# Optimization experiments

Hardware: AMD Instinct MI355X
Metric: run time of the kernel (lower is better)

Reference implementation:

```python
import jax, jax.numpy as jnp
import numpy as np

B = 256          # games in flight
BS = 19          # board side
N2 = BS * BS     # 361 points
M = N2 * 10      # history_factor = 10 -> max moves = 3610


def setup_inputs() -> dict:
    key = jax.random.key(0)
    k = jax.random.split(key, 8)
    legal_mask = jax.random.bernoulli(k[0], 0.5, (B, BS, BS))
    # captures are sparse: few stones captured per candidate move
    capture_stone_mask = jax.random.bernoulli(k[1], 0.02, (B, N2, N2))
    current_player = jax.random.randint(k[2], (B,), 0, 2, dtype=jnp.int32)
    zpos = jax.random.randint(k[3], (N2, 3), 0, 2**31 - 1, dtype=jnp.int32)
    current_hash = jax.random.randint(k[4], (B,), 0, 2**31 - 1, dtype=jnp.int32)
    hash_history = jax.random.randint(k[5], (B, M), 0, 2**31 - 1, dtype=jnp.int32)
    move_count = jax.random.randint(k[6], (B,), 0, M, dtype=jnp.int32)
    logits = jax.random.normal(k[7], (B, BS, BS), dtype=jnp.float32)
    return dict(legal_mask=legal_mask, capture_stone_mask=capture_stone_mask,
                current_player=current_player, zpos=zpos,
                current_hash=current_hash, hash_history=hash_history,
                move_count=move_count, logits=logits)


def _super_ko_filter(legal_mask, capture_stone_mask, current_player, zpos,
                     current_hash, hash_history, move_count):
    Bb, H, W = legal_mask.shape
    n2 = H * W
    legal_flat = legal_mask.reshape(Bb, n2)                      # (B, N2)
    player = current_player.astype(jnp.int32)                    # (B,)
    zposT = zpos.T                                               # (3, N2)

    # 1) delta for placing the stone: empty-key XOR player-key
    place_old = zposT[0][None, :]                                # (1, N2)
    place_new = zposT[player + 1]                                # (B, N2) gather per-batch
    place_delta = jnp.bitwise_xor(place_old, place_new)          # (B, N2)

    # 2) delta for removing a captured opponent stone at each point
    z_opp = zposT[2 - player]                                    # opp+1 = 2-player, (B, N2)
    D = jnp.bitwise_xor(z_opp, zposT[0][None, :])                # (B, N2)

    # per candidate move, XOR the deltas of all stones it would capture
    sel = jnp.where(capture_stone_mask, D[:, None, :], jnp.int32(0))  # (B, N2, N2)
    cap_delta = jax.lax.reduce(sel, jnp.int32(0), jax.lax.bitwise_xor, (2,))  # (B, N2)

    # 3) post-move hash per candidate
    new_hash = current_hash[:, None] ^ place_delta ^ cap_delta   # (B, N2)

    # 4) reject if post-move hash appears in the (valid prefix of) history
    hist_mask = jnp.arange(hash_history.shape[1])[None, :] < move_count[:, None]  # (B, M)
    eq = (new_hash[:, :, None] == hash_history[:, None, :]) & hist_mask[:, None, :]
    is_repeat = jnp.any(eq, axis=2) & legal_flat                 # (B, N2)

    return legal_mask & ~is_repeat.reshape(Bb, H, W)


def reference(legal_mask, capture_stone_mask, current_player, zpos,
              current_hash, hash_history, move_count, logits):
    final_mask = _super_ko_filter(legal_mask, capture_stone_mask, current_player,
                                  zpos, current_hash, hash_history, move_count)
    # downstream use of the filtered mask: mask policy logits
    return jnp.where(final_mask, logits, jnp.float32(-1e9))
```

## Files before the change

### kernel.cpp

```cpp
#include <hip/hip_runtime.h>
#include <stdint.h>


#define GO_B     256
#define GO_N2    361
#define GO_M     3610
#define GO_SLABB (GO_N2 * GO_N2 * 4)
#define TBL      1024
#define NTHR     1024
#define DEPTH    8

__global__ __launch_bounds__(NTHR)
void superko_kernel(const int*   __restrict__ legal,
                    const int*   __restrict__ cap,
                    const int*   __restrict__ player,
                    const int*   __restrict__ zpos,
                    const int*   __restrict__ chash,
                    const int*   __restrict__ hist,
                    const int*   __restrict__ mcount,
                    const float* __restrict__ logits,
                    float*       __restrict__ out)
{
    __shared__ uint32_t Dl[GO_N2];
    __shared__ uint32_t capx[GO_N2];
    __shared__ uint32_t pd[GO_N2];
    __shared__ uint32_t thash[TBL];
    __shared__ int      tidx[TBL];
    __shared__ uint8_t  rep[GO_N2];
    __shared__ uint8_t  leg[GO_N2];

    const int b   = blockIdx.x;
    const int tid = threadIdx.x;
    const int p   = player[b];

    for (int i = tid; i < GO_N2; i += NTHR) {
        uint32_t z0 = (uint32_t)zpos[i * 3 + 0];
        uint32_t zp = (uint32_t)zpos[i * 3 + 1 + p];
        uint32_t zo = (uint32_t)zpos[i * 3 + 2 - p];
        Dl[i]   = zo ^ z0;
        pd[i]   = z0 ^ zp;
        capx[i] = 0u;
        rep[i]  = 0u;
        leg[i]  = legal[(size_t)b * GO_N2 + i] != 0;
    }
    for (int s = tid; s < TBL; s += NTHR) tidx[s] = -1;
    __syncthreads();

    {
        uintptr_t p0   = (uintptr_t)cap + (size_t)b * GO_SLABB;
        uintptr_t a0   = p0 & ~(uintptr_t)15;
        const uint32_t lead   = (uint32_t)(p0 - a0);
        const uint32_t nchunk = (lead + GO_SLABB + 15u) >> 4;
        const uint4* __restrict__ src = (const uint4*)a0;

        for (uint32_t cb = 0; cb < nchunk; cb += NTHR * DEPTH) {
            uint4 w[DEPTH];
            #pragma unroll
            for (int k = 0; k < DEPTH; ++k) {
                uint32_t c = cb + (uint32_t)tid + (uint32_t)k * NTHR;
                uint4 z; z.x = 0u; z.y = 0u; z.z = 0u; z.w = 0u;
                w[k] = (c < nchunk) ? src[c] : z;
            }
            #pragma unroll
            for (int k = 0; k < DEPTH; ++k) {
                uint4 ww = w[k];
                if ((ww.x | ww.y | ww.z | ww.w) == 0u) continue;
                uint32_t base = (cb + (uint32_t)tid + (uint32_t)k * NTHR) * 16u - lead;
                uint32_t dw[4] = { ww.x, ww.y, ww.z, ww.w };
                #pragma unroll
                for (int d = 0; d < 4; ++d) {
                    if (dw[d] != 0u) {
                        uint32_t f = base + (uint32_t)(d * 4);
                        if (f < (uint32_t)GO_SLABB) {
                            uint32_t e = f >> 2;
                            uint32_t i = e / 361u;
                            uint32_t j = e - i * 361u;
                            atomicXor(&capx[i], Dl[j]);
                        }
                    }
                }
            }
        }
    }
    __syncthreads();

    const uint32_t ch = (uint32_t)chash[b];
    for (int i = tid; i < GO_N2; i += NTHR) {
        uint32_t nh = ch ^ pd[i] ^ capx[i];
        if (leg[i]) {
            uint32_t s = nh & (TBL - 1);
            while (true) {
                int prev = atomicCAS(&tidx[s], -1, i);
                if (prev == -1) { thash[s] = nh; break; }
                s = (s + 1) & (TBL - 1);
            }
        }
    }
    __syncthreads();

    const int mc = mcount[b];
    for (int m = tid; m < mc; m += NTHR) {
        uint32_t h = (uint32_t)hist[(size_t)b * GO_M + m];
        uint32_t s = h & (TBL - 1);
        while (tidx[s] != -1) {
            if (thash[s] == h) rep[tidx[s]] = 1u;
            s = (s + 1) & (TBL - 1);
        }
    }
    __syncthreads();

    for (int i = tid; i < GO_N2; i += NTHR) {
        bool keep = leg[i] && !rep[i];
        out[(size_t)b * GO_N2 + i] =
            keep ? logits[(size_t)b * GO_N2 + i] : -1.0e9f;
    }
}

extern "C" void kernel_launch(void* const* d_in, const int* in_sizes, int n_in,
                              void* d_out, int out_size, void* d_ws, size_t ws_size,
                              hipStream_t stream) {
    const int*   legal  = (const int*)d_in[0];
    const int*   cap    = (const int*)d_in[1];
    const int*   player = (const int*)d_in[2];
    const int*   zpos   = (const int*)d_in[3];
    const int*   chash  = (const int*)d_in[4];
    const int*   hist   = (const int*)d_in[5];
    const int*   mcount = (const int*)d_in[6];
    const float* logits = (const float*)d_in[7];
    float*       outp   = (float*)d_out;

    superko_kernel<<<GO_B, NTHR, 0, stream>>>(legal, cap, player, zpos, chash,
                                              hist, mcount, logits, outp);
}
```

Before: 216.8 us.

## Split capture-mask scan across four blocks per game with separate finalize kernel

Each game's capture slab is now scanned by four smaller blocks writing partial XOR accumulators to workspace. A second kernel combines the partials, builds the hash table and checks history. This is meant to raise occupancy and memory-level parallelism beyond one block per game. It adds a second launch and a workspace round-trip.

```diff
diff --git a/kernel.cpp b/kernel.cpp
--- a/kernel.cpp
+++ b/kernel.cpp
@@ -6,24 +6,88 @@
 #define GO_N2    361
 #define GO_M     3610
 #define GO_SLABB (GO_N2 * GO_N2 * 4)
+#define NSPLIT   4
+#define ATHR     512
+#define BTHR     512
 #define TBL      1024
-#define NTHR     1024
 #define DEPTH    8
 
-__global__ __launch_bounds__(NTHR)
-void superko_kernel(const int*   __restrict__ legal,
-                    const int*   __restrict__ cap,
-                    const int*   __restrict__ player,
-                    const int*   __restrict__ zpos,
-                    const int*   __restrict__ chash,
-                    const int*   __restrict__ hist,
-                    const int*   __restrict__ mcount,
-                    const float* __restrict__ logits,
-                    float*       __restrict__ out)
+__global__ __launch_bounds__(ATHR, 8)
+void scan_kernel(const int* __restrict__ cap,
+                 const int* __restrict__ player,
+                 const int* __restrict__ zpos,
+                 uint32_t*  __restrict__ partial)
 {
     __shared__ uint32_t Dl[GO_N2];
     __shared__ uint32_t capx[GO_N2];
-    __shared__ uint32_t pd[GO_N2];
+
+    const int b   = blockIdx.x >> 2;
+    const int q   = blockIdx.x & 3;
+    const int tid = threadIdx.x;
+    const int p   = player[b];
+
+    for (int i = tid; i < GO_N2; i += ATHR) {
+        uint32_t z0 = (uint32_t)zpos[i * 3 + 0];
+        uint32_t zo = (uint32_t)zpos[i * 3 + 2 - p];
+        Dl[i]   = zo ^ z0;
+        capx[i] = 0u;
+    }
+    __syncthreads();
+
+    uintptr_t p0   = (uintptr_t)cap + (size_t)b * GO_SLABB;
+    uintptr_t a0   = p0 & ~(uintptr_t)15;
+    const uint32_t lead   = (uint32_t)(p0 - a0);
+    const uint32_t nchunk = (lead + GO_SLABB + 15u) >> 4;
+    const uint32_t nq     = (nchunk + NSPLIT - 1) / NSPLIT;
+    const uint32_t c0     = (uint32_t)q * nq;
+    const uint32_t c1     = (c0 + nq < nchunk) ? (c0 + nq) : nchunk;
+    const uint4* __restrict__ src = (const uint4*)a0;
+
+    for (uint32_t cb = c0; cb < c1; cb += ATHR * DEPTH) {
+        uint4 w[DEPTH];
+        #pragma unroll
+        for (int k = 0; k < DEPTH; ++k) {
+            uint32_t c = cb + (uint32_t)tid + (uint32_t)k * ATHR;
+            uint4 z; z.x = 0u; z.y = 0u; z.z = 0u; z.w = 0u;
+            w[k] = (c < c1) ? src[c] : z;
+        }
+        #pragma unroll
+        for (int k = 0; k < DEPTH; ++k) {
+            uint4 ww = w[k];
+            if ((ww.x | ww.y | ww.z | ww.w) == 0u) continue;
+            uint32_t base = (cb + (uint32_t)tid + (uint32_t)k * ATHR) * 16u - lead;
+            uint32_t dw[4] = { ww.x, ww.y, ww.z, ww.w };
+            #pragma unroll
+            for (int d = 0; d < 4; ++d) {
+                if (dw[d] != 0u) {
+                    uint32_t f = base + (uint32_t)(d * 4);
+                    if (f < (uint32_t)GO_SLABB) {
+                        uint32_t e = f >> 2;
+                        uint32_t i = e / 361u;
+                        uint32_t j = e - i * 361u;
+                        atomicXor(&capx[i], Dl[j]);
+                    }
+                }
+            }
+        }
+    }
+    __syncthreads();
+
+    uint32_t* __restrict__ dst = partial + ((size_t)b * NSPLIT + q) * GO_N2;
+    for (int i = tid; i < GO_N2; i += ATHR) dst[i] = capx[i];
+}
+
+__global__ __launch_bounds__(BTHR)
+void finalize_kernel(const int*      __restrict__ legal,
+                     const int*      __restrict__ player,
+                     const int*      __restrict__ zpos,
+                     const int*      __restrict__ chash,
+                     const int*      __restrict__ hist,
+                     const int*      __restrict__ mcount,
+                     const float*    __restrict__ logits,
+                     const uint32_t* __restrict__ partial,
+                     float*          __restrict__ out)
+{
     __shared__ uint32_t thash[TBL];
     __shared__ int      tidx[TBL];
     __shared__ uint8_t  rep[GO_N2];
@@ -32,61 +96,21 @@
     const int b   = blockIdx.x;
     const int tid = threadIdx.x;
     const int p   = player[b];
+    const uint32_t ch = (uint32_t)chash[b];
 
-    for (int i = tid; i < GO_N2; i += NTHR) {
-        uint32_t z0 = (uint32_t)zpos[i * 3 + 0];
-        uint32_t zp = (uint32_t)zpos[i * 3 + 1 + p];
-        uint32_t zo = (uint32_t)zpos[i * 3 + 2 - p];
-        Dl[i]   = zo ^ z0;
-        pd[i]   = z0 ^ zp;
-        capx[i] = 0u;
-        rep[i]  = 0u;
-        leg[i]  = legal[(size_t)b * GO_N2 + i] != 0;
-    }
-    for (int s = tid; s < TBL; s += NTHR) tidx[s] = -1;
-    __syncthreads();
-
-    {
-        uintptr_t p0   = (uintptr_t)cap + (size_t)b * GO_SLABB;
-        uintptr_t a0   = p0 & ~(uintptr_t)15;
-        const uint32_t lead   = (uint32_t)(p0 - a0);
-        const uint32_t nchunk = (lead + GO_SLABB + 15u) >> 4;
-        const uint4* __restrict__ src = (const uint4*)a0;
-
-        for (uint32_t cb = 0; cb < nchunk; cb += NTHR * DEPTH) {
-            uint4 w[DEPTH];
-            #pragma unroll
-            for (int k = 0; k < DEPTH; ++k) {
-                uint32_t c = cb + (uint32_t)tid + (uint32_t)k * NTHR;
-                uint4 z; z.x = 0u; z.y = 0u; z.z = 0u; z.w = 0u;
-                w[k] = (c < nchunk) ? src[c] : z;
-            }
-            #pragma unroll
-            for (int k = 0; k < DEPTH; ++k) {
-                uint4 ww = w[k];
-                if ((ww.x | ww.y | ww.z | ww.w) == 0u) continue;
-                uint32_t base = (cb + (uint32_t)tid + (uint32_t)k * NTHR) * 16u - lead;
-                uint32_t dw[4] = { ww.x, ww.y, ww.z, ww.w };
-                #pragma unroll
-                for (int d = 0; d < 4; ++d) {
-                    if (dw[d] != 0u) {
-                        uint32_t f = base + (uint32_t)(d * 4);
-                        if (f < (uint32_t)GO_SLABB) {
-                            uint32_t e = f >> 2;
-                            uint32_t i = e / 361u;
-                            uint32_t j = e - i * 361u;
-                            atomicXor(&capx[i], Dl[j]);
-                        }
-                    }
-                }
-            }
-        }
+    for (int s = tid; s < TBL; s += BTHR) tidx[s] = -1;
+    for (int i = tid; i < GO_N2; i += BTHR) {
+        rep[i] = 0u;
+        leg[i] = legal[(size_t)b * GO_N2 + i] != 0;
     }
     __syncthreads();
 
-    const uint32_t ch = (uint32_t)chash[b];
-    for (int i = tid; i < GO_N2; i += NTHR) {
-        uint32_t nh = ch ^ pd[i] ^ capx[i];
+    const uint32_t* __restrict__ pp = partial + (size_t)b * NSPLIT * GO_N2;
+    for (int i = tid; i < GO_N2; i += BTHR) {
+        uint32_t z0 = (uint32_t)zpos[i * 3 + 0];
+        uint32_t zp = (uint32_t)zpos[i * 3 + 1 + p];
+        uint32_t cx = pp[i] ^ pp[i + GO_N2] ^ pp[i + 2 * GO_N2] ^ pp[i + 3 * GO_N2];
+        uint32_t nh = ch ^ (z0 ^ zp) ^ cx;
         if (leg[i]) {
             uint32_t s = nh & (TBL - 1);
             while (true) {
@@ -99,7 +123,7 @@
     __syncthreads();
 
     const int mc = mcount[b];
-    for (int m = tid; m < mc; m += NTHR) {
+    for (int m = tid; m < mc; m += BTHR) {
         uint32_t h = (uint32_t)hist[(size_t)b * GO_M + m];
         uint32_t s = h & (TBL - 1);
         while (tidx[s] != -1) {
@@ -109,7 +133,7 @@
     }
     __syncthreads();
 
-    for (int i = tid; i < GO_N2; i += NTHR) {
+    for (int i = tid; i < GO_N2; i += BTHR) {
         bool keep = leg[i] && !rep[i];
         out[(size_t)b * GO_N2 + i] =
             keep ? logits[(size_t)b * GO_N2 + i] : -1.0e9f;
@@ -128,7 +152,9 @@
     const int*   mcount = (const int*)d_in[6];
     const float* logits = (const float*)d_in[7];
     float*       outp   = (float*)d_out;
+    uint32_t*    part   = (uint32_t*)d_ws;
 
-    superko_kernel<<<GO_B, NTHR, 0, stream>>>(legal, cap, player, zpos, chash,
-                                              hist, mcount, logits, outp);
+    scan_kernel<<<GO_B * NSPLIT, ATHR, 0, stream>>>(cap, player, zpos, part);
+    finalize_kernel<<<GO_B, BTHR, 0, stream>>>(legal, player, zpos, chash,
+                                               hist, mcount, logits, part, outp);
 }
```

Measured after the change: 237.0 us. 1.09x slower.
